# Kernel tuning notes

Hardware: AMD Instinct MI355X
Metric: run time of the kernel (lower is better)

Reference implementation:

```python
import jax, jax.numpy as jnp
import numpy as np

S = 8192      # total packed tokens
H = 1152      # hidden size
NH = 16       # heads
HD = 72       # head dim
NSEG = 8      # number of packed (equal-length) sequences
L = S // NSEG # tokens per sequence
SCALE = HD ** -0.5


def setup_inputs() -> dict:
    key = jax.random.key(0)
    ks = jax.random.split(key, 4)
    hidden_states = jax.random.normal(ks[0], (1, S, H), jnp.float32)
    # Real rotary cos/sin per token position within each sequence.
    inv_freq = 1.0 / (10000.0 ** (np.arange(0, HD, 2, dtype=np.float64) / HD))
    freqs = np.outer(np.arange(L, dtype=np.float64), inv_freq)  # [L, HD/2]
    emb = np.concatenate([freqs, freqs], axis=-1)               # [L, HD]
    cos = jnp.asarray(np.tile(np.cos(emb), (NSEG, 1)), jnp.float32)  # [S, HD]
    sin = jnp.asarray(np.tile(np.sin(emb), (NSEG, 1)), jnp.float32)
    Wqkv = jax.random.normal(ks[1], (H, 3 * H), jnp.float32) * (H ** -0.5)
    bqkv = jnp.zeros((3 * H,), jnp.float32)
    Wout = jax.random.normal(ks[2], (H, H), jnp.float32) * (H ** -0.5)
    bout = jnp.zeros((H,), jnp.float32)
    cu_seqlens = jnp.arange(NSEG + 1, dtype=jnp.int32) * L
    return dict(hidden_states=hidden_states, cos=cos, sin=sin,
                Wqkv=Wqkv, bqkv=bqkv, Wout=Wout, bout=bout,
                cu_seqlens=cu_seqlens)


def _rotate_half(x):
    return jnp.concatenate([-x[..., HD // 2:], x[..., :HD // 2]], axis=-1)


def reference(hidden_states, cos, sin, Wqkv, bqkv, Wout, bout, cu_seqlens):
    # QKV projection (fused)
    qkv = hidden_states @ Wqkv + bqkv                 # [1, S, 3H]
    q, k, v = jnp.split(qkv, [H, 2 * H], axis=-1)
    q = q.reshape(1, S, NH, HD)
    k = k.reshape(1, S, NH, HD)
    v = v.reshape(1, S, NH, HD)
    # Inline RoPE on q/k (cos/sin broadcast over heads)
    c = cos[None, :, None, :]
    s = sin[None, :, None, :]
    q = q * c + _rotate_half(q) * s
    k = k * c + _rotate_half(k) * s
    # Varlen (block-diagonal) non-causal attention: equal-length segments
    q = q.reshape(NSEG, L, NH, HD)
    k = k.reshape(NSEG, L, NH, HD)
    v = v.reshape(NSEG, L, NH, HD)
    scores = jnp.einsum('nqhd,nkhd->nhqk', q, k) * SCALE  # [NSEG, NH, L, L]
    probs = jax.nn.softmax(scores, axis=-1)
    ctx = jnp.einsum('nhqk,nkhd->nqhd', probs, v)         # [NSEG, L, NH, HD]
    ctx = ctx.reshape(1, S, H)
    # Output projection
    return ctx @ Wout + bout
```

## Files before the change

kernel.cpp:

```cpp
#include <hip/hip_runtime.h>
#include <hip/hip_fp16.h>
#include <cstdint>

typedef _Float16 half8 __attribute__((ext_vector_type(8)));
typedef _Float16 half4 __attribute__((ext_vector_type(4)));
typedef float floatx4 __attribute__((ext_vector_type(4)));

#define S_TOT 8192
#define H_DIM 1152
#define NHEAD 16
#define HD 72
#define QSTR 96
#define KSTR 104
#define PSTR 76
#define VSTR 76
#define VT_TILE 6080
#define NSEG 8
#define SEGL 1024
#define QSCALE 0.17002324631230988f

__device__ __forceinline__ void gld_lds16(const void* g, void* l) {
  __builtin_amdgcn_global_load_lds((const __attribute__((address_space(1))) void*)g,
                                   (__attribute__((address_space(3))) void*)l, 16, 0, 0);
}

__global__ void cast_f32_f16(const float* __restrict__ in, _Float16* __restrict__ out, int n) {
  int i = (blockIdx.x * 256 + threadIdx.x) * 4;
  if (i < n) {
    float4 v = *(const float4*)(in + i);
    half4 o = { (_Float16)v.x, (_Float16)v.y, (_Float16)v.z, (_Float16)v.w };
    *(half4*)(out + i) = o;
  }
}

__global__ void transpose_cast(const float* __restrict__ W, _Float16* __restrict__ Wt,
                               int R, int C) {
  __shared__ float tile[32][33];
  int tx = threadIdx.x, ty = threadIdx.y;
  int bx = blockIdx.x, by = blockIdx.y;
#pragma unroll
  for (int i = 0; i < 4; ++i)
    tile[ty + i * 8][tx] = W[(size_t)(by * 32 + ty + i * 8) * C + bx * 32 + tx];
  __syncthreads();
#pragma unroll
  for (int i = 0; i < 4; ++i)
    Wt[(size_t)(bx * 32 + ty + i * 8) * R + by * 32 + tx] = (_Float16)tile[tx][ty + i * 8];
}

template <bool OUT_HALF>
__global__ __launch_bounds__(256) void gemm_bt(
    const _Float16* __restrict__ A, const _Float16* __restrict__ Bt,
    const float* __restrict__ bias, float* __restrict__ Cf, _Float16* __restrict__ Ch,
    int M, int N, int K, int NT) {
  __shared__ __align__(16) _Float16 As[128 * 72];
  __shared__ __align__(16) _Float16 Bs[128 * 72];
  const int tid = threadIdx.x;
  const int lane = tid & 63, w = tid >> 6;
  const int quad = lane >> 4, l16 = lane & 15;
  const int wm = w >> 1, wn = w & 1;
  const int id = blockIdx.x;
  const int j = id & 7, k = id >> 3;
  const int nt_ = k % NT, mt_ = (k / NT) * 8 + j;
  const int m0 = mt_ * 128, n0 = nt_ * 128;

  int rowi[5], cci[5];
#pragma unroll
  for (int i = 0; i < 5; ++i) {
    int c = tid + i * 256;
    int r = c / 9, cc = c - r * 9;
    rowi[i] = r;
    cci[i] = (cc == 8) ? 0 : cc;
  }

  floatx4 acc[4][4] = {};

  for (int kt = 0; kt < K; kt += 64) {
    __syncthreads();
#pragma unroll
    for (int i = 0; i < 4; ++i) {
      gld_lds16(A + (size_t)(m0 + rowi[i]) * K + kt + cci[i] * 8, (char*)As + (tid + i * 256) * 16);
      gld_lds16(Bt + (size_t)(n0 + rowi[i]) * K + kt + cci[i] * 8, (char*)Bs + (tid + i * 256) * 16);
    }
    if (tid < 128) {
      gld_lds16(A + (size_t)(m0 + rowi[4]) * K + kt + cci[4] * 8, (char*)As + (tid + 1024) * 16);
      gld_lds16(Bt + (size_t)(n0 + rowi[4]) * K + kt + cci[4] * 8, (char*)Bs + (tid + 1024) * 16);
    }
    __syncthreads();
#pragma unroll
    for (int kk = 0; kk < 2; ++kk) {
      half8 af[4], bf[4];
#pragma unroll
      for (int im = 0; im < 4; ++im)
        af[im] = *(const half8*)&As[(wm * 64 + im * 16 + l16) * 72 + kk * 32 + quad * 8];
#pragma unroll
      for (int in = 0; in < 4; ++in)
        bf[in] = *(const half8*)&Bs[(wn * 64 + in * 16 + l16) * 72 + kk * 32 + quad * 8];
#pragma unroll
      for (int im = 0; im < 4; ++im)
#pragma unroll
        for (int in = 0; in < 4; ++in)
          acc[im][in] = __builtin_amdgcn_mfma_f32_16x16x32_f16(af[im], bf[in], acc[im][in], 0, 0, 0);
    }
  }
#pragma unroll
  for (int im = 0; im < 4; ++im) {
    int m = m0 + wm * 64 + im * 16 + quad * 4;
#pragma unroll
    for (int in = 0; in < 4; ++in) {
      int n = n0 + wn * 64 + in * 16 + l16;
      float b = bias[n];
#pragma unroll
      for (int r = 0; r < 4; ++r) {
        float v = acc[im][in][r] + b;
        if (OUT_HALF) Ch[(size_t)(m + r) * N + n] = (_Float16)v;
        else          Cf[(size_t)(m + r) * N + n] = v;
      }
    }
  }
}

__global__ void rope_scatter(const _Float16* __restrict__ QKV,
                             const float* __restrict__ cosb,
                             const float* __restrict__ sinb,
                             _Float16* __restrict__ Qo, _Float16* __restrict__ Ko) {
  int t = blockIdx.x * 256 + threadIdx.x;
  int l = t & 1023, h = (t >> 10) & 15, n = t >> 14;
  int s = n * SEGL + l;
  const _Float16* q = QKV + (size_t)s * 3456 + h * HD;
  const _Float16* k = q + H_DIM;
  const float* cs = cosb + (size_t)s * HD;
  const float* sn = sinb + (size_t)s * HD;
  size_t qo = (size_t)t * QSTR, ko = (size_t)t * KSTR;
  half8 z = {};
  {
    _Float16 qr[72], qv[72];
#pragma unroll
    for (int i = 0; i < 9; ++i) *(half8*)&qr[8 * i] = *(const half8*)(q + 8 * i);
#pragma unroll
    for (int d = 0; d < 36; ++d) {
      float c0 = cs[d], s0 = sn[d], c1 = cs[d + 36], s1 = sn[d + 36];
      float a = (float)qr[d], b = (float)qr[d + 36];
      qv[d]      = (_Float16)((a * c0 - b * s0) * QSCALE);
      qv[d + 36] = (_Float16)((b * c1 + a * s1) * QSCALE);
    }
#pragma unroll
    for (int i = 0; i < 9; ++i) *(half8*)(Qo + qo + 8 * i) = *(half8*)&qv[8 * i];
#pragma unroll
    for (int i = 9; i < 12; ++i) *(half8*)(Qo + qo + 8 * i) = z;
  }
  {
    _Float16 kr[72], kv[72];
#pragma unroll
    for (int i = 0; i < 9; ++i) *(half8*)&kr[8 * i] = *(const half8*)(k + 8 * i);
#pragma unroll
    for (int d = 0; d < 36; ++d) {
      float c0 = cs[d], s0 = sn[d], c1 = cs[d + 36], s1 = sn[d + 36];
      float a = (float)kr[d], b = (float)kr[d + 36];
      kv[d]      = (_Float16)(a * c0 - b * s0);
      kv[d + 36] = (_Float16)(b * c1 + a * s1);
    }
#pragma unroll
    for (int i = 0; i < 9; ++i) *(half8*)(Ko + ko + 8 * i) = *(half8*)&kv[8 * i];
#pragma unroll
    for (int i = 9; i < 13; ++i) *(half8*)(Ko + ko + 8 * i) = z;
  }
}

__global__ __launch_bounds__(256) void transpose_v(const _Float16* __restrict__ QKV,
                                                   _Float16* __restrict__ Vt) {
  __shared__ __align__(16) _Float16 Vs[64 * 88];
  const int tid = threadIdx.x;
  const int kb = blockIdx.x, h = blockIdx.y, n = blockIdx.z;
  const int s0 = n * SEGL + kb * 64;
  const _Float16* src = QKV + (size_t)s0 * 3456 + 2 * H_DIM + h * HD;
  for (int idx = tid; idx < 576; idx += 256) {
    int key = idx / 9, c = idx - key * 9;
    *(half8*)&Vs[key * 88 + c * 8] = *(const half8*)(src + (size_t)key * 3456 + c * 8);
  }
  __syncthreads();
  _Float16* dst = Vt + (((size_t)(n * NHEAD + h)) * 16 + kb) * VT_TILE;
  for (int idx = tid; idx < 800; idx += 256) {
    int d = idx / 10, c = idx - d * 10;
    if (c < 8) {
      half8 v = {};
      if (d < HD) {
#pragma unroll
        for (int j = 0; j < 8; ++j) v[j] = Vs[(c * 8 + j) * 88 + d];
      } else if (d == HD) {
#pragma unroll
        for (int j = 0; j < 8; ++j) v[j] = (_Float16)1.0f;
      }
      *(half8*)(dst + d * VSTR + c * 8) = v;
    } else if (c == 8) {
      *(half8*)(dst + d * VSTR + 64) = half8{};
    } else {
      *(half4*)(dst + d * VSTR + 72) = half4{};
    }
  }
}

__global__ __launch_bounds__(256, 3) void attn_kernel(
    const _Float16* __restrict__ Qb, const _Float16* __restrict__ Kb,
    const _Float16* __restrict__ Vtb, _Float16* __restrict__ Ctx) {
  __shared__ __align__(16) _Float16 Kt[64 * KSTR];
  __shared__ __align__(16) _Float16 Vt[80 * VSTR];
  __shared__ __align__(16) _Float16 Ps[4 * 16 * PSTR];
  const int tid = threadIdx.x;
  const int lane = tid & 63, w = tid >> 6;
  const int quad = lane >> 4, l16 = lane & 15;
  const int id = blockIdx.x;
  const int hn = id & 127, qb = id >> 7;
  const int h = hn >> 3, n = hn & 7;
  const size_t hseg = (size_t)(n * NHEAD + h);
  const _Float16* Qg = Qb + hseg * SEGL * QSTR;
  const _Float16* Kg = Kb + hseg * SEGL * KSTR;
  const _Float16* Vg = Vtb + hseg * 16 * VT_TILE;

  half8 qf[2][3];
#pragma unroll
  for (int qg = 0; qg < 2; ++qg) {
    int row = qb * 128 + w * 32 + qg * 16 + l16;
#pragma unroll
    for (int kc = 0; kc < 3; ++kc)
      qf[qg][kc] = *(const half8*)(Qg + (size_t)row * QSTR + kc * 32 + quad * 8);
  }
  floatx4 o_acc[2][5] = {};

  for (int kb = 0; kb < SEGL / 64; ++kb) {
    __syncthreads();
    {
      const char* base = (const char*)(Kg + (size_t)kb * 64 * KSTR);
#pragma unroll
      for (int i = 0; i < 3; ++i)
        gld_lds16(base + tid * 16 + i * 4096, (char*)Kt + tid * 16 + i * 4096);
      if (tid < 64)
        gld_lds16(base + 12288 + tid * 16, (char*)Kt + 12288 + tid * 16);
    }
    {
      const char* base = (const char*)(Vg + (size_t)kb * VT_TILE);
#pragma unroll
      for (int i = 0; i < 2; ++i)
        gld_lds16(base + tid * 16 + i * 4096, (char*)Vt + tid * 16 + i * 4096);
      if (tid < 248)
        gld_lds16(base + 8192 + tid * 16, (char*)Vt + 8192 + tid * 16);
    }
    __syncthreads();
    floatx4 sa[2][4] = {};
#pragma unroll
    for (int nt = 0; nt < 4; ++nt) {
      half8 kf[3];
#pragma unroll
      for (int kc = 0; kc < 3; ++kc)
        kf[kc] = *(const half8*)&Kt[(nt * 16 + l16) * KSTR + kc * 32 + quad * 8];
#pragma unroll
      for (int qg = 0; qg < 2; ++qg)
#pragma unroll
        for (int kc = 0; kc < 3; ++kc)
          sa[qg][nt] = __builtin_amdgcn_mfma_f32_16x16x32_f16(kf[kc], qf[qg][kc], sa[qg][nt], 0, 0, 0);
    }
#pragma unroll
    for (int qg = 0; qg < 2; ++qg)
#pragma unroll
      for (int nt = 0; nt < 4; ++nt)
#pragma unroll
        for (int r = 0; r < 4; ++r)
          sa[qg][nt][r] = exp2f(sa[qg][nt][r]);
    half8 vf[2][5];
#pragma unroll
    for (int kc2 = 0; kc2 < 2; ++kc2)
#pragma unroll
      for (int t = 0; t < 5; ++t)
        vf[kc2][t] = *(const half8*)&Vt[(t * 16 + l16) * VSTR + kc2 * 32 + quad * 8];
#pragma unroll
    for (int qg = 0; qg < 2; ++qg) {
      int prow = (w * 16 + l16) * PSTR;
#pragma unroll
      for (int nt = 0; nt < 4; ++nt) {
        half4 ph = { (_Float16)sa[qg][nt][0], (_Float16)sa[qg][nt][1],
                     (_Float16)sa[qg][nt][2], (_Float16)sa[qg][nt][3] };
        *(half4*)&Ps[prow + nt * 16 + quad * 4] = ph;
      }
#pragma unroll
      for (int kc2 = 0; kc2 < 2; ++kc2) {
        half8 pb = *(const half8*)&Ps[(w * 16 + l16) * PSTR + kc2 * 32 + quad * 8];
#pragma unroll
        for (int t = 0; t < 5; ++t)
          o_acc[qg][t] = __builtin_amdgcn_mfma_f32_16x16x32_f16(vf[kc2][t], pb, o_acc[qg][t], 0, 0, 0);
      }
    }
  }
#pragma unroll
  for (int qg = 0; qg < 2; ++qg) {
    float lsum = __shfl(o_acc[qg][4][0], 32 + l16, 64);
    float rl = 1.0f / lsum;
    size_t s2 = (size_t)n * SEGL + qb * 128 + w * 32 + qg * 16 + l16;
#pragma unroll
    for (int t = 0; t < 5; ++t) {
      int d0 = t * 16 + quad * 4;
      if (d0 < HD) {
        half4 hv = { (_Float16)(o_acc[qg][t][0] * rl), (_Float16)(o_acc[qg][t][1] * rl),
                     (_Float16)(o_acc[qg][t][2] * rl), (_Float16)(o_acc[qg][t][3] * rl) };
        *(half4*)&Ctx[s2 * H_DIM + h * HD + d0] = hv;
      }
    }
  }
}

extern "C" void kernel_launch(void* const* d_in, const int* in_sizes, int n_in,
                              void* d_out, int out_size, void* d_ws, size_t ws_size,
                              hipStream_t stream) {
  const float* X    = (const float*)d_in[0];
  const float* cosb = (const float*)d_in[1];
  const float* sinb = (const float*)d_in[2];
  const float* Wqkv = (const float*)d_in[3];
  const float* bqkv = (const float*)d_in[4];
  const float* Wout = (const float*)d_in[5];
  const float* bout = (const float*)d_in[6];
  float* out = (float*)d_out;
  char* ws = (char*)d_ws;

  _Float16* Xb   = (_Float16*)(ws);
  _Float16* Wqt  = (_Float16*)(ws + 18874368);
  _Float16* Wot  = (_Float16*)(ws + 26836992);
  _Float16* QKVb = (_Float16*)(ws + 29491200);
  _Float16* Qb   = (_Float16*)(ws + 86114304);
  _Float16* Kb   = (_Float16*)(ws + 111280128);
  _Float16* Vtb  = (_Float16*)(ws + 138543104);
  _Float16* Ctx  = Xb;

  cast_f32_f16<<<9216, 256, 0, stream>>>(X, Xb, S_TOT * H_DIM);
  transpose_cast<<<dim3(108, 36), dim3(32, 8), 0, stream>>>(Wqkv, Wqt, H_DIM, 3 * H_DIM);
  transpose_cast<<<dim3(36, 36), dim3(32, 8), 0, stream>>>(Wout, Wot, H_DIM, H_DIM);
  gemm_bt<true><<<1728, 256, 0, stream>>>(Xb, Wqt, bqkv, nullptr, QKVb,
                                          S_TOT, 3 * H_DIM, H_DIM, 27);
  rope_scatter<<<512, 256, 0, stream>>>(QKVb, cosb, sinb, Qb, Kb);
  transpose_v<<<dim3(16, 16, 8), 256, 0, stream>>>(QKVb, Vtb);
  attn_kernel<<<1024, 256, 0, stream>>>(Qb, Kb, Vtb, Ctx);
  gemm_bt<false><<<576, 256, 0, stream>>>(Ctx, Wot, bout, out, nullptr,
                                          S_TOT, H_DIM, H_DIM, 9);
}
```

Before: 382.0 us.

## Replace GEMM with 256x256-tile, 512-thread double-buffered pipelined kernel

```diff
diff --git a/kernel.cpp b/kernel.cpp
--- a/kernel.cpp
+++ b/kernel.cpp
@@ -48,72 +48,144 @@
 }
 
 template <bool OUT_HALF>
-__global__ __launch_bounds__(256) void gemm_bt(
+__global__ __launch_bounds__(512, 2) void gemm256(
     const _Float16* __restrict__ A, const _Float16* __restrict__ Bt,
     const float* __restrict__ bias, float* __restrict__ Cf, _Float16* __restrict__ Ch,
-    int M, int N, int K, int NT) {
-  __shared__ __align__(16) _Float16 As[128 * 72];
-  __shared__ __align__(16) _Float16 Bs[128 * 72];
+    int M, int N, int K, int NT, int NWG) {
+  extern __shared__ half8 smem8[];
+  char* smem = (char*)smem8;
   const int tid = threadIdx.x;
-  const int lane = tid & 63, w = tid >> 6;
+  const int lane = tid & 63;
+  const int w = tid >> 6;
   const int quad = lane >> 4, l16 = lane & 15;
-  const int wm = w >> 1, wn = w & 1;
-  const int id = blockIdx.x;
-  const int j = id & 7, k = id >> 3;
-  const int nt_ = k % NT, mt_ = (k / NT) * 8 + j;
-  const int m0 = mt_ * 128, n0 = nt_ * 128;
-
-  int rowi[5], cci[5];
-#pragma unroll
-  for (int i = 0; i < 5; ++i) {
-    int c = tid + i * 256;
-    int r = c / 9, cc = c - r * 9;
-    rowi[i] = r;
-    cci[i] = (cc == 8) ? 0 : cc;
-  }
-
-  floatx4 acc[4][4] = {};
-
-  for (int kt = 0; kt < K; kt += 64) {
-    __syncthreads();
-#pragma unroll
-    for (int i = 0; i < 4; ++i) {
-      gld_lds16(A + (size_t)(m0 + rowi[i]) * K + kt + cci[i] * 8, (char*)As + (tid + i * 256) * 16);
-      gld_lds16(Bt + (size_t)(n0 + rowi[i]) * K + kt + cci[i] * 8, (char*)Bs + (tid + i * 256) * 16);
-    }
-    if (tid < 128) {
-      gld_lds16(A + (size_t)(m0 + rowi[4]) * K + kt + cci[4] * 8, (char*)As + (tid + 1024) * 16);
-      gld_lds16(Bt + (size_t)(n0 + rowi[4]) * K + kt + cci[4] * 8, (char*)Bs + (tid + 1024) * 16);
-    }
-    __syncthreads();
-#pragma unroll
-    for (int kk = 0; kk < 2; ++kk) {
-      half8 af[4], bf[4];
-#pragma unroll
-      for (int im = 0; im < 4; ++im)
-        af[im] = *(const half8*)&As[(wm * 64 + im * 16 + l16) * 72 + kk * 32 + quad * 8];
-#pragma unroll
-      for (int in = 0; in < 4; ++in)
-        bf[in] = *(const half8*)&Bs[(wn * 64 + in * 16 + l16) * 72 + kk * 32 + quad * 8];
-#pragma unroll
-      for (int im = 0; im < 4; ++im)
-#pragma unroll
-        for (int in = 0; in < 4; ++in)
-          acc[im][in] = __builtin_amdgcn_mfma_f32_16x16x32_f16(af[im], bf[in], acc[im][in], 0, 0, 0);
-    }
-  }
-#pragma unroll
-  for (int im = 0; im < 4; ++im) {
-    int m = m0 + wm * 64 + im * 16 + quad * 4;
+  const int wm = w >> 2, wn = w & 3;
+
+  const int orig = blockIdx.x;
+  const int wg = (orig & 7) * (NWG >> 3) + (orig >> 3);
+  const int mt = wg / NT, nt = wg - mt * NT;
+  const int m0 = mt * 256, n0 = nt * 256;
+
+  const _Float16* pA[2];
+  const _Float16* pB[2];
+  char* ldst[2];
+#pragma unroll
+  for (int i = 0; i < 2; ++i) {
+    int c = i * 512 + tid;
+    int r = c >> 2, cs = c & 3;
+    int col = ((cs ^ ((r >> 1) & 3)) << 3);
+    pA[i] = A + (size_t)(m0 + r) * K + col;
+    int br = n0 + r; if (br >= N) br = N - 1;
+    pB[i] = Bt + (size_t)br * K + col;
+    ldst[i] = smem + c * 16;
+  }
+  const int e2 = (l16 >> 1) & 3;
+  const int rsl = (quad ^ e2) << 4;
+  const int aoff = (wm * 128 + l16) * 64 + rsl;
+  const int boff = 32768 + (wn * 64 + l16) * 64 + rsl;
+
+  half8 af[4], bf[4];
+  floatx4 acc[8][4] = {};
+
+#define STA(s, kh, kcol) { \
+  gld_lds16(pA[0] + (kcol) + (kh) * 32, ldst[0] + (s) * 65536 + (kh) * 16384); \
+  gld_lds16(pA[1] + (kcol) + (kh) * 32, ldst[1] + (s) * 65536 + (kh) * 16384); }
+#define STB(s, kh, kcol) { \
+  gld_lds16(pB[0] + (kcol) + (kh) * 32, ldst[0] + (s) * 65536 + 32768 + (kh) * 16384); \
+  gld_lds16(pB[1] + (kcol) + (kh) * 32, ldst[1] + (s) * 65536 + 32768 + (kh) * 16384); }
+#define LDB4(s, kk) { \
+  _Pragma("unroll") for (int in = 0; in < 4; ++in) \
+    bf[in] = *(const half8*)(smem + (s) * 65536 + (kk) * 16384 + boff + in * 1024); }
+#define LDA4(s, kk, imh) { \
+  _Pragma("unroll") for (int j = 0; j < 4; ++j) \
+    af[j] = *(const half8*)(smem + (s) * 65536 + (kk) * 16384 + aoff + ((imh) * 4 + j) * 1024); }
+#define MFMA16(imh) { \
+  __builtin_amdgcn_s_setprio(1); \
+  _Pragma("unroll") for (int j = 0; j < 4; ++j) \
+  _Pragma("unroll") for (int in = 0; in < 4; ++in) \
+    acc[(imh) * 4 + j][in] = \
+      __builtin_amdgcn_mfma_f32_16x16x32_f16(af[j], bf[in], acc[(imh) * 4 + j][in], 0, 0, 0); \
+  __builtin_amdgcn_s_setprio(0); }
+#define BAR() __builtin_amdgcn_s_barrier()
+#define LGKM0() { asm volatile("s_waitcnt lgkmcnt(0)" ::: "memory"); __builtin_amdgcn_sched_barrier(0); }
+#define VMW(n) asm volatile("s_waitcnt vmcnt(" #n ")" ::: "memory")
+
+  STA(0, 0, 0); STB(0, 0, 0);
+  STA(0, 1, 0); STB(0, 1, 0);
+  STA(1, 0, 64); STB(1, 0, 64);
+  VMW(4);
+  BAR();
+
+  const int NI = K >> 7;
+#pragma unroll 1
+  for (int it = 0; it < NI; ++it) {
+    const int kt = it << 7;
+    const bool nl = (it + 1 < NI);
+    LDB4(0, 0); LDA4(0, 0, 0);
+    STA(1, 1, kt + 64);
+    BAR(); LGKM0();
+    MFMA16(0);
+    BAR();
+    LDA4(0, 0, 1);
+    STB(1, 1, kt + 64);
+    BAR(); LGKM0();
+    MFMA16(1);
+    BAR();
+    LDB4(0, 1); LDA4(0, 1, 0);
+    if (nl) STA(0, 0, kt + 128);
+    BAR(); LGKM0();
+    MFMA16(0);
+    BAR();
+    LDA4(0, 1, 1);
+    if (nl) STB(0, 0, kt + 128);
+    BAR(); LGKM0();
+    MFMA16(1);
+    if (nl) { VMW(4); } else { VMW(0); }
+    BAR();
+    LDB4(1, 0); LDA4(1, 0, 0);
+    if (nl) STA(0, 1, kt + 128);
+    BAR(); LGKM0();
+    MFMA16(0);
+    BAR();
+    LDA4(1, 0, 1);
+    if (nl) STB(0, 1, kt + 128);
+    BAR(); LGKM0();
+    MFMA16(1);
+    BAR();
+    LDB4(1, 1); LDA4(1, 1, 0);
+    if (nl) STA(1, 0, kt + 192);
+    BAR(); LGKM0();
+    MFMA16(0);
+    BAR();
+    LDA4(1, 1, 1);
+    if (nl) STB(1, 0, kt + 192);
+    BAR(); LGKM0();
+    MFMA16(1);
+    if (nl) VMW(4);
+    BAR();
+  }
+#undef STA
+#undef STB
+#undef LDB4
+#undef LDA4
+#undef MFMA16
+#undef BAR
+#undef LGKM0
+#undef VMW
+
+#pragma unroll
+  for (int im = 0; im < 8; ++im) {
+    int m = m0 + wm * 128 + im * 16 + quad * 4;
 #pragma unroll
     for (int in = 0; in < 4; ++in) {
       int n = n0 + wn * 64 + in * 16 + l16;
-      float b = bias[n];
-#pragma unroll
-      for (int r = 0; r < 4; ++r) {
-        float v = acc[im][in][r] + b;
-        if (OUT_HALF) Ch[(size_t)(m + r) * N + n] = (_Float16)v;
-        else          Cf[(size_t)(m + r) * N + n] = v;
+      if (n < N) {
+        float b = bias[n];
+#pragma unroll
+        for (int r = 0; r < 4; ++r) {
+          float v = acc[im][in][r] + b;
+          if (OUT_HALF) Ch[(size_t)(m + r) * N + n] = (_Float16)v;
+          else          Cf[(size_t)(m + r) * N + n] = v;
+        }
       }
     }
   }
@@ -328,14 +400,23 @@
   _Float16* Vtb  = (_Float16*)(ws + 138543104);
   _Float16* Ctx  = Xb;
 
+  static bool attr_done = false;
+  if (!attr_done) {
+    hipFuncSetAttribute(reinterpret_cast<const void*>(gemm256<true>),
+                        hipFuncAttributeMaxDynamicSharedMemorySize, 131072);
+    hipFuncSetAttribute(reinterpret_cast<const void*>(gemm256<false>),
+                        hipFuncAttributeMaxDynamicSharedMemorySize, 131072);
+    attr_done = true;
+  }
+
   cast_f32_f16<<<9216, 256, 0, stream>>>(X, Xb, S_TOT * H_DIM);
   transpose_cast<<<dim3(108, 36), dim3(32, 8), 0, stream>>>(Wqkv, Wqt, H_DIM, 3 * H_DIM);
   transpose_cast<<<dim3(36, 36), dim3(32, 8), 0, stream>>>(Wout, Wot, H_DIM, H_DIM);
-  gemm_bt<true><<<1728, 256, 0, stream>>>(Xb, Wqt, bqkv, nullptr, QKVb,
-                                          S_TOT, 3 * H_DIM, H_DIM, 27);
+  gemm256<true><<<448, 512, 131072, stream>>>(Xb, Wqt, bqkv, nullptr, QKVb,
+                                              S_TOT, 3 * H_DIM, H_DIM, 14, 448);
   rope_scatter<<<512, 256, 0, stream>>>(QKVb, cosb, sinb, Qb, Kb);
   transpose_v<<<dim3(16, 16, 8), 256, 0, stream>>>(QKVb, Vtb);
   attn_kernel<<<1024, 256, 0, stream>>>(Qb, Kb, Vtb, Ctx);
-  gemm_bt<false><<<576, 256, 0, stream>>>(Ctx, Wot, bout, out, nullptr,
-                                          S_TOT, H_DIM, H_DIM, 9);
-}
+  gemm256<false><<<160, 512, 131072, stream>>>(Ctx, Wot, bout, out, nullptr,
+                                               S_TOT, H_DIM, H_DIM, 5, 160);
+}
```

Measured after the change: 384.9 us. About the same (+0.7%).
